# Kernel tuning notes

Hardware: AMD Instinct MI355X
Metric: run time of the kernel (lower is better)

Reference implementation:

```python
import jax, jax.numpy as jnp
import numpy as np

NA, NB = 4096, 4096
IN, H, E = 256, 512, 131072
NEG_SLOPE = 0.2


def setup_inputs() -> dict:
    key = jax.random.key(0)
    ks = jax.random.split(key, 32)
    f32 = jnp.float32
    nrm = lambda k, s, sc=0.05: jax.random.normal(k, s, f32) * sc
    inp = {
        'x_A': jax.random.normal(ks[0], (NA, IN), f32),
        'x_B': jax.random.normal(ks[1], (NB, IN), f32),
        'edge_AB': jax.random.randint(ks[2], (2, E), 0, NA, jnp.int32),
        'edge_BA': jax.random.randint(ks[3], (2, E), 0, NB, jnp.int32),
        'W_inA': nrm(ks[4], (H, IN)), 'b_inA': jnp.zeros((H,), f32),
        'W_inB': nrm(ks[5], (H, IN)), 'b_inB': jnp.zeros((H,), f32),
        'W_in2A': nrm(ks[6], (H, IN)), 'b_in2A': jnp.zeros((H,), f32),
        'W_in2B': nrm(ks[7], (H, IN)), 'b_in2B': jnp.zeros((H,), f32),
        'Wg1': nrm(ks[8], (H, H)), 'a_src1': nrm(ks[9], (H,)),
        'a_dst1': nrm(ks[10], (H,)), 'bg1': jnp.zeros((H,), f32),
        'Wg2': nrm(ks[11], (H, H)), 'a_src2': nrm(ks[12], (H,)),
        'a_dst2': nrm(ks[13], (H,)), 'bg2': jnp.zeros((H,), f32),
        'Wqkv': nrm(ks[14], (3 * H, H)), 'bqkv': jnp.zeros((3 * H,), f32),
        'Wo': nrm(ks[15], (H, H)), 'bo': jnp.zeros((H,), f32),
    }
    return inp


def gat_conv(x, src, dst, W, a_src, a_dst, b, n):
    # PyG GATConv, heads=1: linear transform, per-edge additive attention,
    # LeakyReLU + segment softmax over incoming edges of each dst node,
    # scatter-sum of weighted source messages. Self-loops already in src/dst.
    h = x @ W.T                                # [n, H]
    e = jax.nn.leaky_relu((h @ a_src)[src] + (h @ a_dst)[dst], NEG_SLOPE)
    m = jax.ops.segment_max(e, dst, num_segments=n)
    ex = jnp.exp(e - m[dst])
    denom = jax.ops.segment_sum(ex, dst, num_segments=n)
    alpha = ex / denom[dst]                    # [E']
    out = jax.ops.segment_sum(h[src] * alpha[:, None], dst, num_segments=n)
    return out + b


def reference(x_A, x_B, edge_AB, edge_BA, W_inA, b_inA, W_inB, b_inB,
              W_in2A, b_in2A, W_in2B, b_in2B,
              Wg1, a_src1, a_dst1, bg1, Wg2, a_src2, a_dst2, bg2,
              Wqkv, bqkv, Wo, bo):
    na, nb = x_A.shape[0], x_B.shape[0]
    n = na + nb
    l = jnp.concatenate([x_A @ W_inA.T + b_inA, x_B @ W_inB.T + b_inB], 0)
    loops = jnp.arange(n, dtype=edge_AB.dtype)
    # to_homogeneous offsets: A at 0, B at na; add self-loops (PyG default)
    src = jnp.concatenate([edge_AB[0], edge_BA[0] + na, loops])
    dst = jnp.concatenate([edge_AB[1] + na, edge_BA[1], loops])
    l = gat_conv(l, src, dst, Wg1, a_src1, a_dst1, bg1, n)
    l = gat_conv(l, src, dst, Wg2, a_src2, a_dst2, bg2, n)
    # global branch: per-type linear -> dense single-head self-attention over all nodes
    g = jnp.concatenate([x_A @ W_in2A.T + b_in2A, x_B @ W_in2B.T + b_in2B], 0)
    qkv = g @ Wqkv.T + bqkv
    q, k, v = jnp.split(qkv, 3, axis=-1)       # each [n, H]
    scale = 1.0 / jnp.sqrt(jnp.asarray(q.shape[-1], q.dtype))
    attn = jax.nn.softmax((q @ k.T) * scale, axis=-1)  # [n, n]
    g = (attn @ v) @ Wo.T + bo
    z_A = jnp.concatenate([l[:na], g[:na]], axis=1)    # [na, 2H]
    z_B = jnp.concatenate([l[na:], g[na:]], axis=1)    # [nb, 2H]
    return (z_A, z_B)
```

## Files before the change

kernel.cpp:

```cpp
#include <hip/hip_runtime.h>
#include <hip/hip_bf16.h>

#define NA_ 4096
#define NB_ 4096
#define NN_ 8192
#define EE_ 131072
#define NE_ (2*EE_ + NN_)
#define HH_ 512
#define NEG_SLOPE_ 0.2f

typedef __attribute__((ext_vector_type(4))) float f32x4;
typedef __attribute__((ext_vector_type(8))) short s16x8;

__device__ inline unsigned short f2bf(float v) {
    __hip_bfloat16 h = __float2bfloat16(v);
    return __builtin_bit_cast(unsigned short, h);
}
__device__ inline float bf2f(unsigned short u) {
    return __uint_as_float(((unsigned)u) << 16);
}

__device__ inline unsigned fkey(float f) {
    unsigned b = __float_as_uint(f);
    return (b & 0x80000000u) ? ~b : (b | 0x80000000u);
}
__device__ inline float finv(unsigned k) {
    return (k & 0x80000000u) ? __uint_as_float(k & 0x7fffffffu)
                             : __uint_as_float(~k);
}

__device__ inline void edge_sd(int i, const int* __restrict__ eAB,
                               const int* __restrict__ eBA, int& s, int& d) {
    if (i < EE_)            { s = eAB[i];            d = eAB[EE_ + i] + NA_; }
    else if (i < 2 * EE_)   { int j = i - EE_; s = eBA[j] + NA_; d = eBA[EE_ + j]; }
    else                    { s = i - 2 * EE_;       d = s; }
}

struct CvtJob { const float* s; unsigned short* hi; unsigned short* lo; int n4; };
struct CvtJobs { CvtJob j[10]; };

__global__ __launch_bounds__(256) void cvt_all_k(CvtJobs jobs) {
    const CvtJob jb = jobs.j[blockIdx.y];
    int i = blockIdx.x * 256 + threadIdx.x;
    if (i >= jb.n4) return;
    float4 v = ((const float4*)jb.s)[i];
    ushort4 h;
    h.x = f2bf(v.x); h.y = f2bf(v.y); h.z = f2bf(v.z); h.w = f2bf(v.w);
    ((ushort4*)jb.hi)[i] = h;
    if (jb.lo) {
        ushort4 l;
        l.x = f2bf(v.x - bf2f(h.x));
        l.y = f2bf(v.y - bf2f(h.y));
        l.z = f2bf(v.z - bf2f(h.z));
        l.w = f2bf(v.w - bf2f(h.w));
        ((ushort4*)jb.lo)[i] = l;
    }
}

template<int BM, int BN, bool BIAS, typename OutT>
__global__ __launch_bounds__(256) void mgemm_k(
    const unsigned short* __restrict__ A, const unsigned short* __restrict__ B,
    const float* __restrict__ bias, OutT* __restrict__ C,
    int K, int lda, int ldb, int ldc)
{
    constexpr int BK = 32;
    constexpr int WM = BM / 2, WN = BN / 2;
    constexpr int AM = WM / 16, AN = WN / 16;
    constexpr int AISS = BM * 4 / 256, BISS = BN * 4 / 256;
    __shared__ unsigned short sA[BM * BK];
    __shared__ unsigned short sB[BN * BK];
    const int t = threadIdx.x, lane = t & 63, w = t >> 6;
    const int wr = w >> 1, wc = w & 1;
    const int fr = lane & 15, fq = lane >> 4;
    const int bm = blockIdx.y * BM, bn = blockIdx.x * BN;

    f32x4 acc[AM][AN];
    #pragma unroll
    for (int m = 0; m < AM; m++)
        #pragma unroll
        for (int n = 0; n < AN; n++)
            #pragma unroll
            for (int r = 0; r < 4; r++) acc[m][n][r] = 0.f;

    for (int k0 = 0; k0 < K; k0 += BK) {
        __syncthreads();
        #pragma unroll
        for (int i = 0; i < AISS; i++) {
            int slot = i * 256 + t;
            __builtin_amdgcn_global_load_lds(
                (const __attribute__((address_space(1))) unsigned int*)
                    (A + (size_t)(bm + (slot >> 2)) * lda + k0 + (slot & 3) * 8),
                (__attribute__((address_space(3))) unsigned int*)
                    (sA + (i * 256 + w * 64) * 8), 16, 0, 0);
        }
        #pragma unroll
        for (int i = 0; i < BISS; i++) {
            int slot = i * 256 + t;
            __builtin_amdgcn_global_load_lds(
                (const __attribute__((address_space(1))) unsigned int*)
                    (B + (size_t)(bn + (slot >> 2)) * ldb + k0 + (slot & 3) * 8),
                (__attribute__((address_space(3))) unsigned int*)
                    (sB + (i * 256 + w * 64) * 8), 16, 0, 0);
        }
        __syncthreads();
        s16x8 a[AM], b[AN];
        #pragma unroll
        for (int m = 0; m < AM; m++)
            a[m] = *(const s16x8*)&sA[(wr * WM + m * 16 + fr) * BK + fq * 8];
        #pragma unroll
        for (int n = 0; n < AN; n++)
            b[n] = *(const s16x8*)&sB[(wc * WN + n * 16 + fr) * BK + fq * 8];
        #pragma unroll
        for (int m = 0; m < AM; m++)
            #pragma unroll
            for (int n = 0; n < AN; n++)
                acc[m][n] = __builtin_amdgcn_mfma_f32_16x16x32_bf16(a[m], b[n], acc[m][n], 0, 0, 0);
    }

    #pragma unroll
    for (int m = 0; m < AM; m++) {
        const int row = bm + wr * WM + m * 16 + fq * 4;
        #pragma unroll
        for (int n = 0; n < AN; n++) {
            const int col = bn + wc * WN + n * 16 + fr;
            const float bv = BIAS ? bias[col] : 0.f;
            #pragma unroll
            for (int r = 0; r < 4; r++) {
                float v = acc[m][n][r] + bv;
                if constexpr (sizeof(OutT) == 2)
                    C[(size_t)(row + r) * ldc + col] = (OutT)f2bf(v);
                else
                    C[(size_t)(row + r) * ldc + col] = v;
            }
        }
    }
}

__global__ __launch_bounds__(256) void mgemm_qk_k(
    const unsigned short* __restrict__ A, const unsigned short* __restrict__ B,
    unsigned short* __restrict__ C, float* __restrict__ denom)
{
    constexpr int BK = 64;
    __shared__ unsigned short sA[128 * BK];
    __shared__ unsigned short sB[128 * BK];
    const int t = threadIdx.x, lane = t & 63, w = t >> 6;
    const int wr = w >> 1, wc = w & 1;
    const int fr = lane & 15, fq = lane >> 4;
    const int bm = blockIdx.y * 128, bn = blockIdx.x * 128;

    f32x4 acc[4][4];
    #pragma unroll
    for (int m = 0; m < 4; m++)
        #pragma unroll
        for (int n = 0; n < 4; n++)
            #pragma unroll
            for (int r = 0; r < 4; r++) acc[m][n][r] = 0.f;

    for (int k0 = 0; k0 < 512; k0 += BK) {
        __syncthreads();
        #pragma unroll
        for (int i = 0; i < 4; i++) {
            int slot = i * 256 + t;
            __builtin_amdgcn_global_load_lds(
                (const __attribute__((address_space(1))) unsigned int*)
                    (A + (size_t)(bm + (slot >> 3)) * 512 + k0 + (slot & 7) * 8),
                (__attribute__((address_space(3))) unsigned int*)
                    (sA + (i * 256 + w * 64) * 8), 16, 0, 0);
            __builtin_amdgcn_global_load_lds(
                (const __attribute__((address_space(1))) unsigned int*)
                    (B + (size_t)(bn + (slot >> 3)) * 512 + k0 + (slot & 7) * 8),
                (__attribute__((address_space(3))) unsigned int*)
                    (sB + (i * 256 + w * 64) * 8), 16, 0, 0);
        }
        __syncthreads();
        s16x8 a[4][2], b[4][2];
        #pragma unroll
        for (int m = 0; m < 4; m++)
            #pragma unroll
            for (int kk = 0; kk < 2; kk++)
                a[m][kk] = *(const s16x8*)&sA[(wr * 64 + m * 16 + fr) * BK + kk * 32 + fq * 8];
        #pragma unroll
        for (int n = 0; n < 4; n++)
            #pragma unroll
            for (int kk = 0; kk < 2; kk++)
                b[n][kk] = *(const s16x8*)&sB[(wc * 64 + n * 16 + fr) * BK + kk * 32 + fq * 8];
        #pragma unroll
        for (int m = 0; m < 4; m++)
            #pragma unroll
            for (int n = 0; n < 4; n++) {
                acc[m][n] = __builtin_amdgcn_mfma_f32_16x16x32_bf16(a[m][0], b[n][0], acc[m][n], 0, 0, 0);
                acc[m][n] = __builtin_amdgcn_mfma_f32_16x16x32_bf16(a[m][1], b[n][1], acc[m][n], 0, 0, 0);
            }
    }

    #pragma unroll
    for (int m = 0; m < 4; m++) {
        const int row = bm + wr * 64 + m * 16 + fq * 4;
        #pragma unroll
        for (int r = 0; r < 4; r++) {
            float rsum = 0.f;
            #pragma unroll
            for (int n = 0; n < 4; n++) {
                const int col = bn + wc * 64 + n * 16 + fr;
                float p = exp2f(acc[m][n][r]);
                rsum += p;
                C[(size_t)(row + r) * 8192 + col] = f2bf(p);
            }
            rsum += __shfl_xor(rsum, 1);
            rsum += __shfl_xor(rsum, 2);
            rsum += __shfl_xor(rsum, 4);
            rsum += __shfl_xor(rsum, 8);
            if (fr == 0) atomicAdd(&denom[row + r], rsum);
        }
    }
}

template<bool SPLIT>
__global__ __launch_bounds__(256) void mgemm_in_k(
    const unsigned short* __restrict__ xA, const unsigned short* __restrict__ xB,
    const unsigned short* __restrict__ WA, const unsigned short* __restrict__ WB,
    const float* __restrict__ biasA, const float* __restrict__ biasB,
    unsigned short* __restrict__ o1, unsigned short* __restrict__ o2)
{
    constexpr int BK = 32;
    __shared__ unsigned short sA[128 * BK];
    __shared__ unsigned short sB[128 * BK];
    const int t = threadIdx.x, lane = t & 63, w = t >> 6;
    const int wr = w >> 1, wc = w & 1;
    const int fr = lane & 15, fq = lane >> 4;
    const int bm = blockIdx.y * 128, bn = blockIdx.x * 128;
    const bool isB = bm >= NA_;
    const unsigned short* A = isB ? xB : xA;
    const unsigned short* W = isB ? WB : WA;
    const float* bias = isB ? biasB : biasA;
    const int bml = bm - (isB ? NA_ : 0);

    f32x4 acc[4][4];
    #pragma unroll
    for (int m = 0; m < 4; m++)
        #pragma unroll
        for (int n = 0; n < 4; n++)
            #pragma unroll
            for (int r = 0; r < 4; r++) acc[m][n][r] = 0.f;

    for (int k0 = 0; k0 < 256; k0 += BK) {
        __syncthreads();
        #pragma unroll
        for (int i = 0; i < 2; i++) {
            int slot = i * 256 + t;
            __builtin_amdgcn_global_load_lds(
                (const __attribute__((address_space(1))) unsigned int*)
                    (A + (size_t)(bml + (slot >> 2)) * 256 + k0 + (slot & 3) * 8),
                (__attribute__((address_space(3))) unsigned int*)
                    (sA + (i * 256 + w * 64) * 8), 16, 0, 0);
            __builtin_amdgcn_global_load_lds(
                (const __attribute__((address_space(1))) unsigned int*)
                    (W + (size_t)(bn + (slot >> 2)) * 256 + k0 + (slot & 3) * 8),
                (__attribute__((address_space(3))) unsigned int*)
                    (sB + (i * 256 + w * 64) * 8), 16, 0, 0);
        }
        __syncthreads();
        s16x8 a[4], b[4];
        #pragma unroll
        for (int m = 0; m < 4; m++)
            a[m] = *(const s16x8*)&sA[(wr * 64 + m * 16 + fr) * BK + fq * 8];
        #pragma unroll
        for (int n = 0; n < 4; n++)
            b[n] = *(const s16x8*)&sB[(wc * 64 + n * 16 + fr) * BK + fq * 8];
        #pragma unroll
        for (int m = 0; m < 4; m++)
            #pragma unroll
            for (int n = 0; n < 4; n++)
                acc[m][n] = __builtin_amdgcn_mfma_f32_16x16x32_bf16(a[m], b[n], acc[m][n], 0, 0, 0);
    }

    #pragma unroll
    for (int m = 0; m < 4; m++) {
        const int row = bm + wr * 64 + m * 16 + fq * 4;
        #pragma unroll
        for (int n = 0; n < 4; n++) {
            const int col = bn + wc * 64 + n * 16 + fr;
            const float bv = bias[col];
            #pragma unroll
            for (int r = 0; r < 4; r++) {
                float v = acc[m][n][r] + bv;
                unsigned short hi = f2bf(v);
                o1[(size_t)(row + r) * 512 + col] = hi;
                if (SPLIT)
                    o2[(size_t)(row + r) * 512 + col] = f2bf(v - bf2f(hi));
            }
        }
    }
}

__global__ __launch_bounds__(256) void mgemm3_k(
    const unsigned short* __restrict__ Ahi, const unsigned short* __restrict__ Alo,
    const unsigned short* __restrict__ Bhi, const unsigned short* __restrict__ Blo,
    float* __restrict__ C, unsigned short* __restrict__ Cb,
    int K, int lda, int ldb, int ldc)
{
    constexpr int BM = 128, BN = 128, BK = 32;
    __shared__ unsigned short sAh[BM * BK], sAl[BM * BK];
    __shared__ unsigned short sBh[BN * BK], sBl[BN * BK];
    const int t = threadIdx.x, lane = t & 63, w = t >> 6;
    const int wr = w >> 1, wc = w & 1;
    const int fr = lane & 15, fq = lane >> 4;
    const int bm = blockIdx.y * BM, bn = blockIdx.x * BN;

    f32x4 acc[4][4];
    #pragma unroll
    for (int m = 0; m < 4; m++)
        #pragma unroll
        for (int n = 0; n < 4; n++)
            #pragma unroll
            for (int r = 0; r < 4; r++) acc[m][n][r] = 0.f;

    for (int k0 = 0; k0 < K; k0 += BK) {
        __syncthreads();
        #pragma unroll
        for (int i = 0; i < 2; i++) {
            int slot = i * 256 + t;
            size_t ga = (size_t)(bm + (slot >> 2)) * lda + k0 + (slot & 3) * 8;
            size_t gb = (size_t)(bn + (slot >> 2)) * ldb + k0 + (slot & 3) * 8;
            unsigned loff = (unsigned)(i * 256 + w * 64) * 8;
            __builtin_amdgcn_global_load_lds(
                (const __attribute__((address_space(1))) unsigned int*)(Ahi + ga),
                (__attribute__((address_space(3))) unsigned int*)(sAh + loff), 16, 0, 0);
            __builtin_amdgcn_global_load_lds(
                (const __attribute__((address_space(1))) unsigned int*)(Alo + ga),
                (__attribute__((address_space(3))) unsigned int*)(sAl + loff), 16, 0, 0);
            __builtin_amdgcn_global_load_lds(
                (const __attribute__((address_space(1))) unsigned int*)(Bhi + gb),
                (__attribute__((address_space(3))) unsigned int*)(sBh + loff), 16, 0, 0);
            __builtin_amdgcn_global_load_lds(
                (const __attribute__((address_space(1))) unsigned int*)(Blo + gb),
                (__attribute__((address_space(3))) unsigned int*)(sBl + loff), 16, 0, 0);
        }
        __syncthreads();
        s16x8 ah[4], al[4], bh[4], bl[4];
        #pragma unroll
        for (int m = 0; m < 4; m++) {
            int o = (wr * 64 + m * 16 + fr) * BK + fq * 8;
            ah[m] = *(const s16x8*)&sAh[o];
            al[m] = *(const s16x8*)&sAl[o];
        }
        #pragma unroll
        for (int n = 0; n < 4; n++) {
            int o = (wc * 64 + n * 16 + fr) * BK + fq * 8;
            bh[n] = *(const s16x8*)&sBh[o];
            bl[n] = *(const s16x8*)&sBl[o];
        }
        #pragma unroll
        for (int m = 0; m < 4; m++)
            #pragma unroll
            for (int n = 0; n < 4; n++) {
                acc[m][n] = __builtin_amdgcn_mfma_f32_16x16x32_bf16(ah[m], bh[n], acc[m][n], 0, 0, 0);
                acc[m][n] = __builtin_amdgcn_mfma_f32_16x16x32_bf16(ah[m], bl[n], acc[m][n], 0, 0, 0);
                acc[m][n] = __builtin_amdgcn_mfma_f32_16x16x32_bf16(al[m], bh[n], acc[m][n], 0, 0, 0);
            }
    }

    #pragma unroll
    for (int m = 0; m < 4; m++) {
        const int row = bm + wr * 64 + m * 16 + fq * 4;
        #pragma unroll
        for (int n = 0; n < 4; n++) {
            const int col = bn + wc * 64 + n * 16 + fr;
            #pragma unroll
            for (int r = 0; r < 4; r++) {
                float v = acc[m][n][r];
                C[(size_t)(row + r) * ldc + col]  = v;
                Cb[(size_t)(row + r) * 512 + col] = f2bf(v);
            }
        }
    }
}

__global__ __launch_bounds__(256) void mgemm_pv_k(
    const unsigned short* __restrict__ A, const unsigned short* __restrict__ B,
    unsigned short* __restrict__ C, int kseg, size_t segstride)
{
    constexpr int BK = 64;
    __shared__ unsigned short sA[128 * BK];
    __shared__ unsigned short sB[128 * BK];
    const int t = threadIdx.x, lane = t & 63, w = t >> 6;
    const int wr = w >> 1, wc = w & 1;
    const int fr = lane & 15, fq = lane >> 4;
    const int L  = blockIdx.x + (blockIdx.y << 2) + (blockIdx.z << 6);
    const int xs = L >> 7;
    const int ys = (L & 127) & 15;
    const int zs = (L & 127) >> 4;
    const int bm = ys * 128, bn = xs * 128;
    const int kofs = zs * kseg;

    f32x4 acc[4][4];
    #pragma unroll
    for (int m = 0; m < 4; m++)
        #pragma unroll
        for (int n = 0; n < 4; n++)
            #pragma unroll
            for (int r = 0; r < 4; r++) acc[m][n][r] = 0.f;

    for (int k0 = 0; k0 < kseg; k0 += BK) {
        __syncthreads();
        #pragma unroll
        for (int i = 0; i < 4; i++) {
            int slot = i * 256 + t;
            __builtin_amdgcn_global_load_lds(
                (const __attribute__((address_space(1))) unsigned int*)
                    (A + (size_t)(bm + (slot >> 3)) * 8192 + kofs + k0 + (slot & 7) * 8),
                (__attribute__((address_space(3))) unsigned int*)
                    (sA + (i * 256 + w * 64) * 8), 16, 0, 0);
            __builtin_amdgcn_global_load_lds(
                (const __attribute__((address_space(1))) unsigned int*)
                    (B + (size_t)(bn + (slot >> 3)) * 8192 + kofs + k0 + (slot & 7) * 8),
                (__attribute__((address_space(3))) unsigned int*)
                    (sB + (i * 256 + w * 64) * 8), 16, 0, 0);
        }
        __syncthreads();
        s16x8 a[4][2], b[4][2];
        #pragma unroll
        for (int m = 0; m < 4; m++)
            #pragma unroll
            for (int kk = 0; kk < 2; kk++)
                a[m][kk] = *(const s16x8*)&sA[(wr * 64 + m * 16 + fr) * BK + kk * 32 + fq * 8];
        #pragma unroll
        for (int n = 0; n < 4; n++)
            #pragma unroll
            for (int kk = 0; kk < 2; kk++)
                b[n][kk] = *(const s16x8*)&sB[(wc * 64 + n * 16 + fr) * BK + kk * 32 + fq * 8];
        #pragma unroll
        for (int m = 0; m < 4; m++)
            #pragma unroll
            for (int n = 0; n < 4; n++) {
                acc[m][n] = __builtin_amdgcn_mfma_f32_16x16x32_bf16(a[m][0], b[n][0], acc[m][n], 0, 0, 0);
                acc[m][n] = __builtin_amdgcn_mfma_f32_16x16x32_bf16(a[m][1], b[n][1], acc[m][n], 0, 0, 0);
            }
    }

    unsigned short* Cz = C + (size_t)zs * segstride;
    #pragma unroll
    for (int m = 0; m < 4; m++) {
        const int row = bm + wr * 64 + m * 16 + fq * 4;
        #pragma unroll
        for (int n = 0; n < 4; n++) {
            const int col = bn + wc * 64 + n * 16 + fr;
            #pragma unroll
            for (int r = 0; r < 4; r++)
                Cz[(size_t)(row + r) * 512 + col] = f2bf(acc[m][n][r]);
        }
    }
}

__global__ __launch_bounds__(256) void radd_k(const unsigned short* __restrict__ src,
                                              unsigned short* __restrict__ dst,
                                              const float* __restrict__ dn,
                                              int n8, int segs, size_t stride8) {
    int i = blockIdx.x * 256 + threadIdx.x;
    if (i >= n8) return;
    float acc[8] = {0,0,0,0,0,0,0,0};
    for (int s = 0; s < segs; s++) {
        s16x8 v = ((const s16x8*)src)[i + s * stride8];
        #pragma unroll
        for (int j = 0; j < 8; j++) acc[j] += bf2f((unsigned short)v[j]);
    }
    const float rd = 1.0f / dn[i >> 6];
    s16x8 o;
    #pragma unroll
    for (int j = 0; j < 8; j++) o[j] = (short)f2bf(acc[j] * rd);
    ((s16x8*)dst)[i] = o;
}

__global__ __launch_bounds__(256) void mgemm_qkv_k(
    const unsigned short* __restrict__ A, const unsigned short* __restrict__ B,
    const float* __restrict__ bias, float scale,
    unsigned short* __restrict__ qb, unsigned short* __restrict__ kb,
    unsigned short* __restrict__ vb)
{
    constexpr int BM = 128, BN = 128, BK = 32;
    __shared__ unsigned short sA[BM * BK];
    __shared__ unsigned short sB[BN * BK];
    const int t = threadIdx.x, lane = t & 63, w = t >> 6;
    const int wr = w >> 1, wc = w & 1;
    const int fr = lane & 15, fq = lane >> 4;
    const int bm = blockIdx.y * BM, bn = blockIdx.x * BN;

    f32x4 acc[4][4];
    #pragma unroll
    for (int m = 0; m < 4; m++)
        #pragma unroll
        for (int n = 0; n < 4; n++)
            #pragma unroll
            for (int r = 0; r < 4; r++) acc[m][n][r] = 0.f;

    for (int k0 = 0; k0 < 512; k0 += BK) {
        __syncthreads();
        #pragma unroll
        for (int i = 0; i < 2; i++) {
            int slot = i * 256 + t;
            __builtin_amdgcn_global_load_lds(
                (const __attribute__((address_space(1))) unsigned int*)
                    (A + (size_t)(bm + (slot >> 2)) * 512 + k0 + (slot & 3) * 8),
                (__attribute__((address_space(3))) unsigned int*)
                    (sA + (i * 256 + w * 64) * 8), 16, 0, 0);
            __builtin_amdgcn_global_load_lds(
                (const __attribute__((address_space(1))) unsigned int*)
                    (B + (size_t)(bn + (slot >> 2)) * 512 + k0 + (slot & 3) * 8),
                (__attribute__((address_space(3))) unsigned int*)
                    (sB + (i * 256 + w * 64) * 8), 16, 0, 0);
        }
        __syncthreads();
        s16x8 a[4], b[4];
        #pragma unroll
        for (int m = 0; m < 4; m++)
            a[m] = *(const s16x8*)&sA[(wr * 64 + m * 16 + fr) * BK + fq * 8];
        #pragma unroll
        for (int n = 0; n < 4; n++)
            b[n] = *(const s16x8*)&sB[(wc * 64 + n * 16 + fr) * BK + fq * 8];
        #pragma unroll
        for (int m = 0; m < 4; m++)
            #pragma unroll
            for (int n = 0; n < 4; n++)
                acc[m][n] = __builtin_amdgcn_mfma_f32_16x16x32_bf16(a[m], b[n], acc[m][n], 0, 0, 0);
    }

    #pragma unroll
    for (int m = 0; m < 4; m++) {
        const int row = bm + wr * 64 + m * 16 + fq * 4;
        #pragma unroll
        for (int n = 0; n < 4; n++) {
            const int col = bn + wc * 64 + n * 16 + fr;
            const float bv = bias[col];
            #pragma unroll
            for (int r = 0; r < 4; r++) {
                float v = acc[m][n][r] + bv;
                if (col < 512)
                    qb[(size_t)(row + r) * 512 + col] = f2bf(v * scale);
                else if (col < 1024)
                    kb[(size_t)(row + r) * 512 + (col - 512)] = f2bf(v);
                else
                    vb[(size_t)(row + r) * 512 + (col - 1024)] = f2bf(v);
            }
        }
    }
}

__global__ __launch_bounds__(256) void trT_k(const unsigned short* __restrict__ vb,
                                             unsigned short* __restrict__ vT) {
    __shared__ unsigned short s[64][65];
    const int t = threadIdx.x;
    const int rowo = blockIdx.y * 64;
    const int colo = blockIdx.x * 64;
    {
        int r = t >> 2, cg = (t & 3) * 16;
        const s16x8* src = (const s16x8*)(vb + (size_t)(rowo + r) * 512 + colo + cg);
        s16x8 u0 = src[0], u1 = src[1];
        #pragma unroll
        for (int j = 0; j < 8; j++) {
            s[r][cg + j]     = (unsigned short)u0[j];
            s[r][cg + 8 + j] = (unsigned short)u1[j];
        }
    }
    __syncthreads();
    {
        int c = t >> 2, rg = (t & 3) * 16;
        s16x8 o0, o1;
        #pragma unroll
        for (int j = 0; j < 8; j++) {
            o0[j] = (short)s[rg + j][c];
            o1[j] = (short)s[rg + 8 + j][c];
        }
        s16x8* dst = (s16x8*)(vT + (size_t)(colo + c) * 8192 + rowo + rg);
        dst[0] = o0; dst[1] = o1;
    }
}

__global__ __launch_bounds__(256) void node_dots_k(
    const float* __restrict__ h, const float* __restrict__ a_src,
    const float* __restrict__ a_dst, float* __restrict__ as_, float* __restrict__ ad_)
{
    int wid  = (blockIdx.x * 256 + threadIdx.x) >> 6;
    int lane = threadIdx.x & 63;
    if (wid >= NN_) return;
    const float* hr = h + (size_t)wid * HH_;
    float s1 = 0.f, s2 = 0.f;
    #pragma unroll
    for (int j = 0; j < 8; j++) {
        float v = hr[lane + j*64];
        s1 = fmaf(v, a_src[lane + j*64], s1);
        s2 = fmaf(v, a_dst[lane + j*64], s2);
    }
    #pragma unroll
    for (int off = 32; off; off >>= 1) {
        s1 += __shfl_down(s1, off);
        s2 += __shfl_down(s2, off);
    }
    if (lane == 0) { as_[wid] = s1; ad_[wid] = s2; }
}

__global__ void count_deg_k(const int* eAB, const int* eBA, int* deg) {
    int i = blockIdx.x * 256 + threadIdx.x;
    if (i >= NE_) return;
    int s, d; edge_sd(i, eAB, eBA, s, d);
    atomicAdd(&deg[d], 1);
}

__global__ __launch_bounds__(256) void scan_k(const int* __restrict__ deg, int* rowstart) {
    __shared__ int part[256];
    int t = threadIdx.x;
    int base = t * 32;
    int loc[32]; int s = 0;
    #pragma unroll
    for (int j = 0; j < 32; j++) { loc[j] = s; s += deg[base + j]; }
    part[t] = s;
    __syncthreads();
    if (t == 0) {
        int a = 0;
        for (int i = 0; i < 256; i++) { int v = part[i]; part[i] = a; a += v; }
        rowstart[NN_] = a;
    }
    __syncthreads();
    int off = part[t];
    #pragma unroll
    for (int j = 0; j < 32; j++) rowstart[base + j] = off + loc[j];
}

__global__ void fill_csr_k(const int* eAB, const int* eBA,
                           const int* __restrict__ rowstart, int* cursor,
                           int* csr_src, int* pos) {
    int i = blockIdx.x * 256 + threadIdx.x;
    if (i >= NE_) return;
    int s, d; edge_sd(i, eAB, eBA, s, d);
    int p = atomicAdd(&cursor[d], 1);
    int slot = rowstart[d] + p;
    csr_src[slot] = s;
    pos[i] = slot;
}

__global__ void edge_pass1_k(const int* eAB, const int* eBA,
                             const float* __restrict__ as_, const float* __restrict__ ad_,
                             float* evals, unsigned* mkey) {
    int i = blockIdx.x * 256 + threadIdx.x;
    if (i >= NE_) return;
    int s, d; edge_sd(i, eAB, eBA, s, d);
    float e = as_[s] + ad_[d];
    e = (e >= 0.f) ? e : NEG_SLOPE_ * e;
    evals[i] = e;
    atomicMax(&mkey[d], fkey(e));
}

__global__ void edge_pass2_k(const int* eAB, const int* eBA,
                             const unsigned* __restrict__ mkey,
                             const float* __restrict__ evals,
                             const int* __restrict__ pos,
                             float* __restrict__ evs, float* denom) {
    int i = blockIdx.x * 256 + threadIdx.x;
    if (i >= NE_) return;
    int s, d; edge_sd(i, eAB, eBA, s, d);
    float m = finv(mkey[d]);
    float ex = expf(evals[i] - m);
    evs[pos[i]] = ex;
    atomicAdd(&denom[d], ex);
}

template<bool SPLIT>
__global__ __launch_bounds__(256) void gat_agg_k(
    const int* __restrict__ rowstart, const int* __restrict__ csr_src,
    const float* __restrict__ evs, const float* __restrict__ denom,
    const unsigned short* __restrict__ hb, const float* __restrict__ bias,
    float* __restrict__ outF, int ldo,
    unsigned short* __restrict__ outHi, unsigned short* __restrict__ outLo)
{
    int wid  = (blockIdx.x * 256 + threadIdx.x) >> 6;
    int lane = threadIdx.x & 63;
    if (wid >= NN_) return;
    float acc[8] = {0.f,0.f,0.f,0.f,0.f,0.f,0.f,0.f};
    int beg = rowstart[wid], end = rowstart[wid + 1];
    float rden = 1.0f / denom[wid];
    for (int p = beg; p < end; p++) {
        int s = csr_src[p];
        float alpha = evs[p] * rden;
        s16x8 hv = *(const s16x8*)(hb + (size_t)s * HH_ + lane * 8);
        #pragma unroll
        for (int j = 0; j < 8; j++)
            acc[j] = fmaf(alpha, bf2f((unsigned short)hv[j]), acc[j]);
    }
    #pragma unroll
    for (int j = 0; j < 8; j++) acc[j] += bias[lane * 8 + j];
    if (SPLIT) {
        s16x8 hi, lo;
        #pragma unroll
        for (int j = 0; j < 8; j++) {
            unsigned short h = f2bf(acc[j]);
            hi[j] = (short)h;
            lo[j] = (short)f2bf(acc[j] - bf2f(h));
        }
        *(s16x8*)(outHi + (size_t)wid * HH_ + lane * 8) = hi;
        *(s16x8*)(outLo + (size_t)wid * HH_ + lane * 8) = lo;
    } else {
        float* o = outF + (size_t)wid * ldo + lane * 8;
        *(float4*)(o)     = make_float4(acc[0], acc[1], acc[2], acc[3]);
        *(float4*)(o + 4) = make_float4(acc[4], acc[5], acc[6], acc[7]);
    }
}

extern "C" void kernel_launch(void* const* d_in, const int* in_sizes, int n_in,
                              void* d_out, int out_size, void* d_ws, size_t ws_size,
                              hipStream_t stream)
{
    const float* x_A    = (const float*)d_in[0];
    const float* x_B    = (const float*)d_in[1];
    const int*   eAB    = (const int*)d_in[2];
    const int*   eBA    = (const int*)d_in[3];
    const float* W_inA  = (const float*)d_in[4];  const float* b_inA  = (const float*)d_in[5];
    const float* W_inB  = (const float*)d_in[6];  const float* b_inB  = (const float*)d_in[7];
    const float* W_in2A = (const float*)d_in[8];  const float* b_in2A = (const float*)d_in[9];
    const float* W_in2B = (const float*)d_in[10]; const float* b_in2B = (const float*)d_in[11];
    const float* Wg1    = (const float*)d_in[12]; const float* a_src1 = (const float*)d_in[13];
    const float* a_dst1 = (const float*)d_in[14]; const float* bg1    = (const float*)d_in[15];
    const float* Wg2    = (const float*)d_in[16]; const float* a_src2 = (const float*)d_in[17];
    const float* a_dst2 = (const float*)d_in[18]; const float* bg2    = (const float*)d_in[19];
    const float* Wqkv   = (const float*)d_in[20]; const float* bqkv   = (const float*)d_in[21];
    const float* Wo     = (const float*)d_in[22]; const float* bo     = (const float*)d_in[23];

    float* out = (float*)d_out;

    char* base = (char*)d_ws;
    size_t off = 0;
    auto alloc = [&](size_t nb) -> char* {
        char* p = base + off;
        off = (off + nb + 255) & ~(size_t)255;
        return p;
    };

    float*          bufA  = (float*)alloc((size_t)NN_ * 512 * 4);
    float*          bufB  = (float*)alloc((size_t)NN_ * 512 * 4);
    float*          bufC  = (float*)alloc((size_t)NN_ * 512 * 4);
    float*          as_   = (float*)alloc(NN_ * 4);
    float*          ad_   = (float*)alloc(NN_ * 4);
    unsigned*       mkey  = (unsigned*)alloc(NN_ * 4);
    float*          denom = (float*)alloc(NN_ * 4);
    int*            deg   = (int*)alloc(NN_ * 4);
    int*            cursor= (int*)alloc(NN_ * 4);
    float*          cdn   = (float*)alloc(NN_ * 4);
    int*            rowst = (int*)alloc((NN_ + 1) * 4);
    float*          evals = (float*)alloc((size_t)NE_ * 4);
    int*            csrs  = (int*)alloc((size_t)NE_ * 4);
    int*            pos   = (int*)alloc((size_t)NE_ * 4);
    float*          evs   = (float*)alloc((size_t)NE_ * 4);
    unsigned short* xbA   = (unsigned short*)alloc((size_t)NA_ * 256 * 2);
    unsigned short* xbB   = (unsigned short*)alloc((size_t)NB_ * 256 * 2);
    unsigned short* WbinA = (unsigned short*)alloc((size_t)512 * 256 * 2);
    unsigned short* WbinB = (unsigned short*)alloc((size_t)512 * 256 * 2);
    unsigned short* Wbin2A= (unsigned short*)alloc((size_t)512 * 256 * 2);
    unsigned short* Wbin2B= (unsigned short*)alloc((size_t)512 * 256 * 2);
    unsigned short* Wbqkv = (unsigned short*)alloc((size_t)1536 * 512 * 2);
    unsigned short* Wbo   = (unsigned short*)alloc((size_t)512 * 512 * 2);
    unsigned short* Wg1hi = (unsigned short*)alloc((size_t)512 * 512 * 2);
    unsigned short* Wg1lo = (unsigned short*)alloc((size_t)512 * 512 * 2);
    unsigned short* Wg2hi = (unsigned short*)alloc((size_t)512 * 512 * 2);
    unsigned short* Wg2lo = (unsigned short*)alloc((size_t)512 * 512 * 2);
    unsigned short* qb    = (unsigned short*)alloc((size_t)NN_ * 512 * 2);
    unsigned short* kb    = (unsigned short*)alloc((size_t)NN_ * 512 * 2);
    unsigned short* vT    = (unsigned short*)alloc((size_t)512 * NN_ * 2);
    unsigned short* ab    = (unsigned short*)alloc((size_t)NN_ * 512 * 2);

    unsigned short* hb = vT;
    unsigned short* gb = (unsigned short*)bufC;
    unsigned short* vb = gb + (size_t)NN_ * 512;
    unsigned short* Sb = (unsigned short*)bufA;
    unsigned short* pv = (unsigned short*)bufC;

    const int R = 2048, SEGS = 8, KSEG = 8192 / SEGS;
    const int EG = (NE_ + 255) / 256;
    const float scale2 = 0.044194173824159216f * 1.4426950408889634f;

    CvtJobs jobs;
    jobs.j[0] = { x_A,    xbA,    nullptr, NA_ * 256 / 4 };
    jobs.j[1] = { x_B,    xbB,    nullptr, NB_ * 256 / 4 };
    jobs.j[2] = { W_inA,  WbinA,  nullptr, 512 * 256 / 4 };
    jobs.j[3] = { W_inB,  WbinB,  nullptr, 512 * 256 / 4 };
    jobs.j[4] = { W_in2A, Wbin2A, nullptr, 512 * 256 / 4 };
    jobs.j[5] = { W_in2B, Wbin2B, nullptr, 512 * 256 / 4 };
    jobs.j[6] = { Wqkv,   Wbqkv,  nullptr, 1536 * 512 / 4 };
    jobs.j[7] = { Wo,     Wbo,    nullptr, 512 * 512 / 4 };
    jobs.j[8] = { Wg1,    Wg1hi,  Wg1lo,   512 * 512 / 4 };
    jobs.j[9] = { Wg2,    Wg2hi,  Wg2lo,   512 * 512 / 4 };
    cvt_all_k<<<dim3(NA_ * 256 / 4 / 256, 10), 256, 0, stream>>>(jobs);

    hipMemsetAsync(mkey, 0, (size_t)NN_ * 4 * 5, stream);

    count_deg_k<<<EG, 256, 0, stream>>>(eAB, eBA, deg);
    scan_k<<<1, 256, 0, stream>>>(deg, rowst);
    fill_csr_k<<<EG, 256, 0, stream>>>(eAB, eBA, rowst, cursor, csrs, pos);

    mgemm_in_k<true><<<dim3(4, 64), 256, 0, stream>>>(
        xbA, xbB, WbinA, WbinB, b_inA, b_inB, qb, kb);
    mgemm3_k<<<dim3(4, 64), 256, 0, stream>>>(qb, kb, Wg1hi, Wg1lo,
                                              bufB, hb, 512, 512, 512, 512);
    node_dots_k<<<NN_/4, 256, 0, stream>>>(bufB, a_src1, a_dst1, as_, ad_);
    edge_pass1_k<<<EG, 256, 0, stream>>>(eAB, eBA, as_, ad_, evals, mkey);
    edge_pass2_k<<<EG, 256, 0, stream>>>(eAB, eBA, mkey, evals, pos, evs, denom);
    gat_agg_k<true><<<NN_/4, 256, 0, stream>>>(rowst, csrs, evs, denom,
                                               hb, bg1, nullptr, 0, qb, kb);
    mgemm3_k<<<dim3(4, 64), 256, 0, stream>>>(qb, kb, Wg2hi, Wg2lo,
                                              bufB, hb, 512, 512, 512, 512);
    node_dots_k<<<NN_/4, 256, 0, stream>>>(bufB, a_src2, a_dst2, as_, ad_);
    hipMemsetAsync(mkey, 0, NN_ * 8, stream);
    edge_pass1_k<<<EG, 256, 0, stream>>>(eAB, eBA, as_, ad_, evals, mkey);
    edge_pass2_k<<<EG, 256, 0, stream>>>(eAB, eBA, mkey, evals, pos, evs, denom);
    gat_agg_k<false><<<NN_/4, 256, 0, stream>>>(rowst, csrs, evs, denom,
                                                hb, bg2, out, 1024, nullptr, nullptr);

    mgemm_in_k<false><<<dim3(4, 64), 256, 0, stream>>>(
        xbA, xbB, Wbin2A, Wbin2B, b_in2A, b_in2B, gb, nullptr);
    mgemm_qkv_k<<<dim3(12, 64), 256, 0, stream>>>(gb, Wbqkv, bqkv, scale2, qb, kb, vb);
    trT_k<<<dim3(8, 128), 256, 0, stream>>>(vb, vT);
    for (int c0 = 0; c0 < 8192; c0 += R) {
        float* dn = cdn + c0;
        mgemm_qk_k<<<dim3(64, R/128), 256, 0, stream>>>(
            qb + (size_t)c0 * 512, kb, Sb, dn);
        mgemm_pv_k<<<dim3(4, R/128, SEGS), 256, 0, stream>>>(
            Sb, vT, pv, KSEG, (size_t)R * 512);
        radd_k<<<(R*512/8 + 255)/256, 256, 0, stream>>>(
            pv, ab + (size_t)c0 * 512, dn, R*512/8, SEGS, (size_t)R*512/8);
    }
    mgemm_k<128,128,true,float><<<dim3(4, 64), 256, 0, stream>>>(
        ab, Wbo, bo, out + 512, 512, 512, 512, 1024);
}
```

Baseline: 651.3 us.

## Retile QK GEMM to 256x256, swizzle LDS, and drop fp32 GAT output

The QK^T score kernel moves from 128x128 tiles with 256 threads to 256x256 tiles with 512 threads, so each loaded tile of Q and K is reused more. The QK and PV kernels both switch to an XOR-swizzled LDS layout to avoid bank conflicts on the MFMA operand reads. mgemm3 no longer writes an fp32 copy of h, and node_dots now reads the bf16 copy instead, which saves a large store and read. In exchange the attention-logit dot products lose some precision, and the QK launch grid is hardcoded to assume a particular chunk size R.

```diff
diff --git a/kernel.cpp b/kernel.cpp
--- a/kernel.cpp
+++ b/kernel.cpp
@@ -136,21 +136,21 @@
     }
 }
 
-__global__ __launch_bounds__(256) void mgemm_qk_k(
+__global__ __launch_bounds__(512) void mgemm_qk_k(
     const unsigned short* __restrict__ A, const unsigned short* __restrict__ B,
     unsigned short* __restrict__ C, float* __restrict__ denom)
 {
     constexpr int BK = 64;
-    __shared__ unsigned short sA[128 * BK];
-    __shared__ unsigned short sB[128 * BK];
+    __shared__ unsigned short sA[256 * BK];
+    __shared__ unsigned short sB[256 * BK];
     const int t = threadIdx.x, lane = t & 63, w = t >> 6;
-    const int wr = w >> 1, wc = w & 1;
+    const int wr = w >> 2, wc = w & 3;
     const int fr = lane & 15, fq = lane >> 4;
-    const int bm = blockIdx.y * 128, bn = blockIdx.x * 128;
-
-    f32x4 acc[4][4];
-    #pragma unroll
-    for (int m = 0; m < 4; m++)
+    const int bm = blockIdx.y * 256, bn = blockIdx.x * 256;
+
+    f32x4 acc[8][4];
+    #pragma unroll
+    for (int m = 0; m < 8; m++)
         #pragma unroll
         for (int n = 0; n < 4; n++)
             #pragma unroll
@@ -160,57 +160,60 @@
         __syncthreads();
         #pragma unroll
         for (int i = 0; i < 4; i++) {
-            int slot = i * 256 + t;
-            __builtin_amdgcn_global_load_lds(
-                (const __attribute__((address_space(1))) unsigned int*)
-                    (A + (size_t)(bm + (slot >> 3)) * 512 + k0 + (slot & 7) * 8),
-                (__attribute__((address_space(3))) unsigned int*)
-                    (sA + (i * 256 + w * 64) * 8), 16, 0, 0);
-            __builtin_amdgcn_global_load_lds(
-                (const __attribute__((address_space(1))) unsigned int*)
-                    (B + (size_t)(bn + (slot >> 3)) * 512 + k0 + (slot & 7) * 8),
-                (__attribute__((address_space(3))) unsigned int*)
-                    (sB + (i * 256 + w * 64) * 8), 16, 0, 0);
-        }
-        __syncthreads();
-        s16x8 a[4][2], b[4][2];
-        #pragma unroll
-        for (int m = 0; m < 4; m++)
-            #pragma unroll
-            for (int kk = 0; kk < 2; kk++)
-                a[m][kk] = *(const s16x8*)&sA[(wr * 64 + m * 16 + fr) * BK + kk * 32 + fq * 8];
-        #pragma unroll
-        for (int n = 0; n < 4; n++)
-            #pragma unroll
-            for (int kk = 0; kk < 2; kk++)
-                b[n][kk] = *(const s16x8*)&sB[(wc * 64 + n * 16 + fr) * BK + kk * 32 + fq * 8];
-        #pragma unroll
-        for (int m = 0; m < 4; m++)
+            int s = i * 512 + t;
+            int row = s >> 3, cc = s & 7;
+            int gc = k0 + ((cc ^ (row & 7)) << 3);
+            __builtin_amdgcn_global_load_lds(
+                (const __attribute__((address_space(1))) unsigned int*)
+                    (A + (size_t)(bm + row) * 512 + gc),
+                (__attribute__((address_space(3))) unsigned int*)
+                    (sA + (i * 512 + w * 64) * 8), 16, 0, 0);
+            __builtin_amdgcn_global_load_lds(
+                (const __attribute__((address_space(1))) unsigned int*)
+                    (B + (size_t)(bn + row) * 512 + gc),
+                (__attribute__((address_space(3))) unsigned int*)
+                    (sB + (i * 512 + w * 64) * 8), 16, 0, 0);
+        }
+        __syncthreads();
+        #pragma unroll
+        for (int kk = 0; kk < 2; kk++) {
+            s16x8 a[8], b[4];
+            #pragma unroll
+            for (int m = 0; m < 8; m++) {
+                int row = wr * 128 + m * 16 + fr;
+                a[m] = *(const s16x8*)&sA[row * BK + (((kk * 4 + fq) ^ (row & 7)) << 3)];
+            }
             #pragma unroll
             for (int n = 0; n < 4; n++) {
-                acc[m][n] = __builtin_amdgcn_mfma_f32_16x16x32_bf16(a[m][0], b[n][0], acc[m][n], 0, 0, 0);
-                acc[m][n] = __builtin_amdgcn_mfma_f32_16x16x32_bf16(a[m][1], b[n][1], acc[m][n], 0, 0, 0);
+                int row = wc * 64 + n * 16 + fr;
+                b[n] = *(const s16x8*)&sB[row * BK + (((kk * 4 + fq) ^ (row & 7)) << 3)];
             }
-    }
-
-    #pragma unroll
-    for (int m = 0; m < 4; m++) {
-        const int row = bm + wr * 64 + m * 16 + fq * 4;
+            #pragma unroll
+            for (int m = 0; m < 8; m++)
+                #pragma unroll
+                for (int n = 0; n < 4; n++)
+                    acc[m][n] = __builtin_amdgcn_mfma_f32_16x16x32_bf16(a[m], b[n], acc[m][n], 0, 0, 0);
+        }
+    }
+
+    #pragma unroll
+    for (int m = 0; m < 8; m++) {
         #pragma unroll
         for (int r = 0; r < 4; r++) {
+            const int row = bm + wr * 128 + m * 16 + fq * 4 + r;
             float rsum = 0.f;
             #pragma unroll
             for (int n = 0; n < 4; n++) {
                 const int col = bn + wc * 64 + n * 16 + fr;
                 float p = exp2f(acc[m][n][r]);
                 rsum += p;
-                C[(size_t)(row + r) * 8192 + col] = f2bf(p);
+                C[(size_t)row * 8192 + col] = f2bf(p);
             }
             rsum += __shfl_xor(rsum, 1);
             rsum += __shfl_xor(rsum, 2);
             rsum += __shfl_xor(rsum, 4);
             rsum += __shfl_xor(rsum, 8);
-            if (fr == 0) atomicAdd(&denom[row + r], rsum);
+            if (fr == 0) atomicAdd(&denom[row], rsum);
         }
     }
 }
@@ -296,8 +299,7 @@
 __global__ __launch_bounds__(256) void mgemm3_k(
     const unsigned short* __restrict__ Ahi, const unsigned short* __restrict__ Alo,
     const unsigned short* __restrict__ Bhi, const unsigned short* __restrict__ Blo,
-    float* __restrict__ C, unsigned short* __restrict__ Cb,
-    int K, int lda, int ldb, int ldc)
+    unsigned short* __restrict__ Cb, int K, int lda, int ldb)
 {
     constexpr int BM = 128, BN = 128, BK = 32;
     __shared__ unsigned short sAh[BM * BK], sAl[BM * BK];
@@ -367,11 +369,8 @@
         for (int n = 0; n < 4; n++) {
             const int col = bn + wc * 64 + n * 16 + fr;
             #pragma unroll
-            for (int r = 0; r < 4; r++) {
-                float v = acc[m][n][r];
-                C[(size_t)(row + r) * ldc + col]  = v;
-                Cb[(size_t)(row + r) * 512 + col] = f2bf(v);
-            }
+            for (int r = 0; r < 4; r++)
+                Cb[(size_t)(row + r) * 512 + col] = f2bf(acc[m][n][r]);
         }
     }
 }
@@ -405,37 +404,40 @@
         __syncthreads();
         #pragma unroll
         for (int i = 0; i < 4; i++) {
-            int slot = i * 256 + t;
-            __builtin_amdgcn_global_load_lds(
-                (const __attribute__((address_space(1))) unsigned int*)
-                    (A + (size_t)(bm + (slot >> 3)) * 8192 + kofs + k0 + (slot & 7) * 8),
+            int s = i * 256 + t;
+            int row = s >> 3, cc = s & 7;
+            int gc = kofs + k0 + ((cc ^ (row & 7)) << 3);
+            __builtin_amdgcn_global_load_lds(
+                (const __attribute__((address_space(1))) unsigned int*)
+                    (A + (size_t)(bm + row) * 8192 + gc),
                 (__attribute__((address_space(3))) unsigned int*)
                     (sA + (i * 256 + w * 64) * 8), 16, 0, 0);
             __builtin_amdgcn_global_load_lds(
                 (const __attribute__((address_space(1))) unsigned int*)
-                    (B + (size_t)(bn + (slot >> 3)) * 8192 + kofs + k0 + (slot & 7) * 8),
+                    (B + (size_t)(bn + row) * 8192 + gc),
                 (__attribute__((address_space(3))) unsigned int*)
                     (sB + (i * 256 + w * 64) * 8), 16, 0, 0);
         }
         __syncthreads();
-        s16x8 a[4][2], b[4][2];
-        #pragma unroll
-        for (int m = 0; m < 4; m++)
-            #pragma unroll
-            for (int kk = 0; kk < 2; kk++)
-                a[m][kk] = *(const s16x8*)&sA[(wr * 64 + m * 16 + fr) * BK + kk * 32 + fq * 8];
-        #pragma unroll
-        for (int n = 0; n < 4; n++)
-            #pragma unroll
-            for (int kk = 0; kk < 2; kk++)
-                b[n][kk] = *(const s16x8*)&sB[(wc * 64 + n * 16 + fr) * BK + kk * 32 + fq * 8];
-        #pragma unroll
-        for (int m = 0; m < 4; m++)
+        #pragma unroll
+        for (int kk = 0; kk < 2; kk++) {
+            s16x8 a[4], b[4];
+            #pragma unroll
+            for (int m = 0; m < 4; m++) {
+                int row = wr * 64 + m * 16 + fr;
+                a[m] = *(const s16x8*)&sA[row * BK + (((kk * 4 + fq) ^ (row & 7)) << 3)];
+            }
             #pragma unroll
             for (int n = 0; n < 4; n++) {
-                acc[m][n] = __builtin_amdgcn_mfma_f32_16x16x32_bf16(a[m][0], b[n][0], acc[m][n], 0, 0, 0);
-                acc[m][n] = __builtin_amdgcn_mfma_f32_16x16x32_bf16(a[m][1], b[n][1], acc[m][n], 0, 0, 0);
+                int row = wc * 64 + n * 16 + fr;
+                b[n] = *(const s16x8*)&sB[row * BK + (((kk * 4 + fq) ^ (row & 7)) << 3)];
             }
+            #pragma unroll
+            for (int m = 0; m < 4; m++)
+                #pragma unroll
+                for (int n = 0; n < 4; n++)
+                    acc[m][n] = __builtin_amdgcn_mfma_f32_16x16x32_bf16(a[m], b[n], acc[m][n], 0, 0, 0);
+        }
     }
 
     unsigned short* Cz = C + (size_t)zs * segstride;
@@ -576,19 +578,19 @@
 }
 
 __global__ __launch_bounds__(256) void node_dots_k(
-    const float* __restrict__ h, const float* __restrict__ a_src,
+    const unsigned short* __restrict__ hb, const float* __restrict__ a_src,
     const float* __restrict__ a_dst, float* __restrict__ as_, float* __restrict__ ad_)
 {
     int wid  = (blockIdx.x * 256 + threadIdx.x) >> 6;
     int lane = threadIdx.x & 63;
     if (wid >= NN_) return;
-    const float* hr = h + (size_t)wid * HH_;
+    s16x8 hv = *(const s16x8*)(hb + (size_t)wid * HH_ + lane * 8);
     float s1 = 0.f, s2 = 0.f;
     #pragma unroll
     for (int j = 0; j < 8; j++) {
-        float v = hr[lane + j*64];
-        s1 = fmaf(v, a_src[lane + j*64], s1);
-        s2 = fmaf(v, a_dst[lane + j*64], s2);
+        float v = bf2f((unsigned short)hv[j]);
+        s1 = fmaf(v, a_src[lane * 8 + j], s1);
+        s2 = fmaf(v, a_dst[lane * 8 + j], s2);
     }
     #pragma unroll
     for (int off = 32; off; off >>= 1) {
@@ -797,15 +799,15 @@
     mgemm_in_k<true><<<dim3(4, 64), 256, 0, stream>>>(
         xbA, xbB, WbinA, WbinB, b_inA, b_inB, qb, kb);
     mgemm3_k<<<dim3(4, 64), 256, 0, stream>>>(qb, kb, Wg1hi, Wg1lo,
-                                              bufB, hb, 512, 512, 512, 512);
-    node_dots_k<<<NN_/4, 256, 0, stream>>>(bufB, a_src1, a_dst1, as_, ad_);
+                                              hb, 512, 512, 512);
+    node_dots_k<<<NN_/4, 256, 0, stream>>>(hb, a_src1, a_dst1, as_, ad_);
     edge_pass1_k<<<EG, 256, 0, stream>>>(eAB, eBA, as_, ad_, evals, mkey);
     edge_pass2_k<<<EG, 256, 0, stream>>>(eAB, eBA, mkey, evals, pos, evs, denom);
     gat_agg_k<true><<<NN_/4, 256, 0, stream>>>(rowst, csrs, evs, denom,
                                                hb, bg1, nullptr, 0, qb, kb);
     mgemm3_k<<<dim3(4, 64), 256, 0, stream>>>(qb, kb, Wg2hi, Wg2lo,
-                                              bufB, hb, 512, 512, 512, 512);
-    node_dots_k<<<NN_/4, 256, 0, stream>>>(bufB, a_src2, a_dst2, as_, ad_);
+                                              hb, 512, 512, 512);
+    node_dots_k<<<NN_/4, 256, 0, stream>>>(hb, a_src2, a_dst2, as_, ad_);
     hipMemsetAsync(mkey, 0, NN_ * 8, stream);
     edge_pass1_k<<<EG, 256, 0, stream>>>(eAB, eBA, as_, ad_, evals, mkey);
     edge_pass2_k<<<EG, 256, 0, stream>>>(eAB, eBA, mkey, evals, pos, evs, denom);
@@ -818,7 +820,7 @@
     trT_k<<<dim3(8, 128), 256, 0, stream>>>(vb, vT);
     for (int c0 = 0; c0 < 8192; c0 += R) {
         float* dn = cdn + c0;
-        mgemm_qk_k<<<dim3(64, R/128), 256, 0, stream>>>(
+        mgemm_qk_k<<<dim3(32, 8), 512, 0, stream>>>(
             qb + (size_t)c0 * 512, kb, Sb, dn);
         mgemm_pv_k<<<dim3(4, R/128, SEGS), 256, 0, stream>>>(
             Sb, vT, pv, KSEG, (size_t)R * 512);
```

Result: faster. 611.4 us (-6.1%).
